# Optimization experiments

Hardware: AMD Instinct MI355X
Metric: run time of the kernel (lower is better)

## Reference

```python
import jax, jax.numpy as jnp
import numpy as np

V = 32          # number_variables
DEG = 12        # degree
ORDER = 3       # spline_order (cubic)
N_BASIS = DEG + ORDER - 1  # 14, rows of params
LO, HI = -15.0, 15.0       # polynomial_range[:, 0]
EPS = 1e-6


def make_knots():
    dist = (HI - LO) / (DEG - 1)
    k = DEG + 2 * ORDER
    return jnp.linspace(LO - ORDER * dist, HI + ORDER * dist, k, dtype=jnp.float32)


def bspline_basis(x, knots, order):
    # x: [N, P] -> basis: [N, P, N_BASIS] via Cox-de Boor recursion (Naive_Basis)
    xk = x[..., None]
    b = ((xk >= knots[:-1]) & (xk < knots[1:])).astype(x.dtype)  # degree-0, [N,P,K-1]
    t = knots
    for k in range(1, order + 1):
        left = (xk - t[:-(k + 1)]) / (t[k:-1] - t[:-(k + 1)])
        right = (t[k + 1:] - xk) / (t[k + 1:] - t[1:-k])
        b = left * b[..., :-1] + right * b[..., 1:]
    return b  # [N, P, K-1-order] == [N, P, N_BASIS]


def setup_inputs() -> dict:
    key = jax.random.key(0)
    k1, k2 = jax.random.split(key)
    num_lambdas = V * (V - 1) // 2  # 496
    inp = jax.random.normal(k1, (16384, V), dtype=jnp.float32)
    log_d = jnp.zeros((16384, V), dtype=jnp.float32)
    params = 0.001 * jnp.ones((N_BASIS, num_lambdas), dtype=jnp.float32)
    return {"input": inp, "log_d": log_d, "params": params}


def reference(input, log_d, params):
    n = input.shape[0]
    knots = make_knots()
    rows, cols = np.tril_indices(V, -1)  # matches torch.tril_indices(V, V, offset=-1)
    rows = jnp.asarray(rows); cols = jnp.asarray(cols)
    # clamp into half-open spline support for valid degree-0 basis
    x = jnp.clip(input, LO, HI - EPS)
    xs = x[:, cols]                                  # [N, P] per-pair covariate values
    basis = bspline_basis(xs, knots, ORDER)          # [N, P, N_BASIS]
    lam = jnp.einsum('npk,kp->np', basis, params)    # [N, P] lambda values
    # lower-triangular lambda matrix: identity + strict lower entries
    lm = jnp.broadcast_to(jnp.eye(V, dtype=input.dtype), (n, V, V))
    lm = lm.at[:, rows, cols].set(lam)
    out = jnp.einsum('nvc,nc->nv', lm, input)        # bmm(lambda_matrix, input)
    # ridge penalties on spline coefficients (penalize_towards=0)
    d2 = jnp.diff(params, n=2, axis=0)
    d1 = jnp.diff(params, n=1, axis=0)
    second_pen = jnp.sum(d2 ** 2)
    first_pen = jnp.sum(d1 ** 2)
    param_pen = jnp.sum(params ** 2)
    return out, lm, second_pen, first_pen, param_pen
```

## Files before the change

kernel.cpp:

```cpp
#include <hip/hip_runtime.h>

#define VDIM   32
#define NPAIR  496
#define NBASIS 14
#define NPARAM (NBASIS * NPAIR)
#define ROWS   16
#define SPS    15

typedef float f32x4 __attribute__((ext_vector_type(4)));

__device__ __forceinline__ float spline_u(float xi) {
    const float invd = 11.0f / 30.0f;
    float x = fminf(fmaxf(xi, -15.0f), 15.0f - 1e-6f);
    return x * invd + 8.5f;
}

__global__ __launch_bounds__(256) void Decorrelation_35270271435435_kernel(
    const float* __restrict__ input,
    const float* __restrict__ params,
    float* __restrict__ out,
    float* __restrict__ lm,
    float* __restrict__ pens,
    int N)
{
    __shared__ float sp[NPAIR * SPS];
    __shared__ float xin[ROWS][VDIM];
    __shared__ f32x4 wgt4[ROWS][VDIM];

    const int tid = threadIdx.x;
    const int n0  = blockIdx.x * ROWS;

    {
        const f32x4* p4 = (const f32x4*)params;
        for (int i4 = tid; i4 < NPARAM / 4; i4 += 256) {
            const f32x4 val = p4[i4];
            const int base = i4 * 4;
            #pragma unroll
            for (int e = 0; e < 4; ++e) {
                const int idx = base + e;
                const int k = idx / NPAIR;
                const int p = idx - k * NPAIR;
                sp[p * SPS + k] = val[e];
            }
        }
    }

    #pragma unroll
    for (int it = 0; it < 2; ++it) {
        const int item = tid + it * 256;
        const int r = item >> 5, c = item & 31;
        const int n = n0 + r;
        const float xi = (n < N) ? input[n * VDIM + c] : 0.0f;
        xin[r][c] = xi;
        const float u  = spline_u(xi);
        float fi = floorf(u);
        fi = fminf(fmaxf(fi, 3.0f), 13.0f);
        const float uu  = u - fi;
        const float om  = 1.0f - uu;
        const float uu2 = uu * uu, uu3 = uu2 * uu;
        const float sixth = 1.0f / 6.0f;
        f32x4 w;
        w[0] = om * om * om * sixth;
        w[1] = (3.0f * uu3 - 6.0f * uu2 + 4.0f) * sixth;
        w[2] = (-3.0f * uu3 + 3.0f * uu2 + 3.0f * uu + 1.0f) * sixth;
        w[3] = uu3 * sixth;
        wgt4[r][((c & 3) << 3) | (c >> 2)] = w;
    }
    __syncthreads();

    const int v  = tid >> 3;
    const int t  = tid & 7;
    const int c0 = t << 2;
    int  pb[4];
    bool low[4], dia[4];
    #pragma unroll
    for (int j = 0; j < 4; ++j) {
        const int c = c0 + j;
        low[j] = (c < v);
        dia[j] = (c == v);
        pb[j]  = ((v * (v - 1)) / 2 + c) * SPS;
    }

    const int rlim = (N - n0 < ROWS) ? (N - n0) : ROWS;
    float* lmp = lm + (size_t)n0 * (VDIM * VDIM) + tid * 4;

    #pragma unroll 4
    for (int r = 0; r < ROWS; ++r, lmp += VDIM * VDIM) {
        const f32x4 x4 = *(const f32x4*)&xin[r][c0];
        float vals[4];
        float partial = 0.0f;
        #pragma unroll
        for (int j = 0; j < 4; ++j) {
            float val = 0.0f;
            if (dia[j]) {
                val = 1.0f;
            } else if (low[j]) {
                const float u = spline_u(x4[j]);
                float fi = floorf(u);
                fi = fminf(fmaxf(fi, 3.0f), 13.0f);
                const int k0 = (int)fi - 3;
                const float* q = &sp[pb[j] + k0];
                const f32x4 w = wgt4[r][(j << 3) | t];
                val = w[0] * q[0] + w[1] * q[1] + w[2] * q[2] + w[3] * q[3];
            }
            vals[j] = val;
            partial += val * x4[j];
        }
        if (r < rlim) {
            const f32x4 f4 = { vals[0], vals[1], vals[2], vals[3] };
            __builtin_nontemporal_store(f4, (f32x4*)lmp);
            partial += __shfl_down(partial, 4, 8);
            partial += __shfl_down(partial, 2, 8);
            partial += __shfl_down(partial, 1, 8);
            if (t == 0) out[(size_t)(n0 + r) * VDIM + v] = partial;
        }
    }

    if (blockIdx.x == 0) {
        float s2 = 0.0f, s1 = 0.0f, spn = 0.0f;
        for (int p = tid; p < NPAIR; p += 256) {
            const float* q = &sp[p * SPS];
            float a[NBASIS];
            #pragma unroll
            for (int k = 0; k < NBASIS; ++k) { a[k] = q[k]; spn += a[k] * a[k]; }
            #pragma unroll
            for (int k = 0; k < NBASIS - 1; ++k) {
                const float d = a[k + 1] - a[k];
                s1 += d * d;
            }
            #pragma unroll
            for (int k = 0; k < NBASIS - 2; ++k) {
                const float d = a[k + 2] - 2.0f * a[k + 1] + a[k];
                s2 += d * d;
            }
        }
        #pragma unroll
        for (int off = 32; off > 0; off >>= 1) {
            s2  += __shfl_down(s2, off);
            s1  += __shfl_down(s1, off);
            spn += __shfl_down(spn, off);
        }
        __shared__ float wsum[3][4];
        const int lane = tid & 63, wid = tid >> 6;
        if (lane == 0) { wsum[0][wid] = s2; wsum[1][wid] = s1; wsum[2][wid] = spn; }
        __syncthreads();
        if (tid == 0) {
            pens[0] = wsum[0][0] + wsum[0][1] + wsum[0][2] + wsum[0][3];
            pens[1] = wsum[1][0] + wsum[1][1] + wsum[1][2] + wsum[1][3];
            pens[2] = wsum[2][0] + wsum[2][1] + wsum[2][2] + wsum[2][3];
        }
    }
}

extern "C" void kernel_launch(void* const* d_in, const int* in_sizes, int n_in,
                              void* d_out, int out_size, void* d_ws, size_t ws_size,
                              hipStream_t stream) {
    const float* input  = (const float*)d_in[0];
    const float* params = (const float*)d_in[2];
    const int N = in_sizes[0] / VDIM;

    float* out  = (float*)d_out;
    float* lm   = out + (size_t)N * VDIM;
    float* pens = lm + (size_t)N * VDIM * VDIM;

    const int nb = (N + ROWS - 1) / ROWS;
    Decorrelation_35270271435435_kernel<<<nb, 256, 0, stream>>>(
        input, params, out, lm, pens, N);
}
```

Measured before the change: 89.79 us.

## Double block size and compute spline weights inline per element

Blocks grow to 512 threads, so two row groups work on interleaved rows and each thread handles half as many rows. The shared-memory staging of inputs and precomputed cubic B-spline weights is removed. Each thread now reads its input row directly from global memory and computes the weights in registers, which drops one LDS pass and its associated buffers. The cost is redundant weight computation and an unchanged per-block params load into shared memory. That load is now amortised over fewer rows per thread but shared across more threads.

Result: slower. 92.66 us (+3.2%).

```diff
diff --git a/kernel.cpp b/kernel.cpp
--- a/kernel.cpp
+++ b/kernel.cpp
@@ -5,6 +5,7 @@
 #define NBASIS 14
 #define NPARAM (NBASIS * NPAIR)
 #define ROWS   16
+#define BLK    512
 #define SPS    15
 
 typedef float f32x4 __attribute__((ext_vector_type(4)));
@@ -15,7 +16,7 @@
     return x * invd + 8.5f;
 }
 
-__global__ __launch_bounds__(256) void Decorrelation_35270271435435_kernel(
+__global__ __launch_bounds__(BLK, 8) void Decorrelation_35270271435435_kernel(
     const float* __restrict__ input,
     const float* __restrict__ params,
     float* __restrict__ out,
@@ -24,15 +25,14 @@
     int N)
 {
     __shared__ float sp[NPAIR * SPS];
-    __shared__ float xin[ROWS][VDIM];
-    __shared__ f32x4 wgt4[ROWS][VDIM];
+    __shared__ float wsum[3][8];
 
     const int tid = threadIdx.x;
     const int n0  = blockIdx.x * ROWS;
 
     {
         const f32x4* p4 = (const f32x4*)params;
-        for (int i4 = tid; i4 < NPARAM / 4; i4 += 256) {
+        for (int i4 = tid; i4 < NPARAM / 4; i4 += BLK) {
             const f32x4 val = p4[i4];
             const int base = i4 * 4;
             #pragma unroll
@@ -44,31 +44,10 @@
             }
         }
     }
-
-    #pragma unroll
-    for (int it = 0; it < 2; ++it) {
-        const int item = tid + it * 256;
-        const int r = item >> 5, c = item & 31;
-        const int n = n0 + r;
-        const float xi = (n < N) ? input[n * VDIM + c] : 0.0f;
-        xin[r][c] = xi;
-        const float u  = spline_u(xi);
-        float fi = floorf(u);
-        fi = fminf(fmaxf(fi, 3.0f), 13.0f);
-        const float uu  = u - fi;
-        const float om  = 1.0f - uu;
-        const float uu2 = uu * uu, uu3 = uu2 * uu;
-        const float sixth = 1.0f / 6.0f;
-        f32x4 w;
-        w[0] = om * om * om * sixth;
-        w[1] = (3.0f * uu3 - 6.0f * uu2 + 4.0f) * sixth;
-        w[2] = (-3.0f * uu3 + 3.0f * uu2 + 3.0f * uu + 1.0f) * sixth;
-        w[3] = uu3 * sixth;
-        wgt4[r][((c & 3) << 3) | (c >> 2)] = w;
-    }
     __syncthreads();
 
-    const int v  = tid >> 3;
+    const int g  = tid >> 8;
+    const int v  = (tid >> 3) & 31;
     const int t  = tid & 7;
     const int c0 = t << 2;
     int  pb[4];
@@ -81,12 +60,14 @@
         pb[j]  = ((v * (v - 1)) / 2 + c) * SPS;
     }
 
-    const int rlim = (N - n0 < ROWS) ? (N - n0) : ROWS;
-    float* lmp = lm + (size_t)n0 * (VDIM * VDIM) + tid * 4;
+    float* lmp0 = lm + (size_t)(n0 + g) * (VDIM * VDIM) + (tid & 255) * 4;
 
-    #pragma unroll 4
-    for (int r = 0; r < ROWS; ++r, lmp += VDIM * VDIM) {
-        const f32x4 x4 = *(const f32x4*)&xin[r][c0];
+    #pragma unroll 2
+    for (int i = 0; i < ROWS / 2; ++i) {
+        const int r = g + (i << 1);
+        const int n = n0 + r;
+        if (n >= N) break;
+        const f32x4 x4 = *(const f32x4*)&input[(size_t)n * VDIM + c0];
         float vals[4];
         float partial = 0.0f;
         #pragma unroll
@@ -98,27 +79,33 @@
                 const float u = spline_u(x4[j]);
                 float fi = floorf(u);
                 fi = fminf(fmaxf(fi, 3.0f), 13.0f);
+                const float uu  = u - fi;
+                const float om  = 1.0f - uu;
+                const float uu2 = uu * uu, uu3 = uu2 * uu;
+                const float sixth = 1.0f / 6.0f;
+                const float w0 = om * om * om * sixth;
+                const float w1 = (3.0f * uu3 - 6.0f * uu2 + 4.0f) * sixth;
+                const float w2 = (-3.0f * uu3 + 3.0f * uu2 + 3.0f * uu + 1.0f) * sixth;
+                const float w3 = uu3 * sixth;
                 const int k0 = (int)fi - 3;
                 const float* q = &sp[pb[j] + k0];
-                const f32x4 w = wgt4[r][(j << 3) | t];
-                val = w[0] * q[0] + w[1] * q[1] + w[2] * q[2] + w[3] * q[3];
+                val = w0 * q[0] + w1 * q[1] + w2 * q[2] + w3 * q[3];
             }
             vals[j] = val;
             partial += val * x4[j];
         }
-        if (r < rlim) {
-            const f32x4 f4 = { vals[0], vals[1], vals[2], vals[3] };
-            __builtin_nontemporal_store(f4, (f32x4*)lmp);
-            partial += __shfl_down(partial, 4, 8);
-            partial += __shfl_down(partial, 2, 8);
-            partial += __shfl_down(partial, 1, 8);
-            if (t == 0) out[(size_t)(n0 + r) * VDIM + v] = partial;
-        }
+        const f32x4 f4 = { vals[0], vals[1], vals[2], vals[3] };
+        __builtin_nontemporal_store(f4, (f32x4*)(lmp0 + (size_t)(i << 1) * (VDIM * VDIM)));
+
+        partial += __shfl_down(partial, 4, 8);
+        partial += __shfl_down(partial, 2, 8);
+        partial += __shfl_down(partial, 1, 8);
+        if (t == 0) out[(size_t)n * VDIM + v] = partial;
     }
 
     if (blockIdx.x == 0) {
         float s2 = 0.0f, s1 = 0.0f, spn = 0.0f;
-        for (int p = tid; p < NPAIR; p += 256) {
+        for (int p = tid; p < NPAIR; p += BLK) {
             const float* q = &sp[p * SPS];
             float a[NBASIS];
             #pragma unroll
@@ -140,14 +127,14 @@
             s1  += __shfl_down(s1, off);
             spn += __shfl_down(spn, off);
         }
-        __shared__ float wsum[3][4];
         const int lane = tid & 63, wid = tid >> 6;
         if (lane == 0) { wsum[0][wid] = s2; wsum[1][wid] = s1; wsum[2][wid] = spn; }
         __syncthreads();
         if (tid == 0) {
-            pens[0] = wsum[0][0] + wsum[0][1] + wsum[0][2] + wsum[0][3];
-            pens[1] = wsum[1][0] + wsum[1][1] + wsum[1][2] + wsum[1][3];
-            pens[2] = wsum[2][0] + wsum[2][1] + wsum[2][2] + wsum[2][3];
+            float r0 = 0.f, r1 = 0.f, r2 = 0.f;
+            #pragma unroll
+            for (int w = 0; w < 8; ++w) { r0 += wsum[0][w]; r1 += wsum[1][w]; r2 += wsum[2][w]; }
+            pens[0] = r0; pens[1] = r1; pens[2] = r2;
         }
     }
 }
@@ -164,6 +151,6 @@
     float* pens = lm + (size_t)N * VDIM * VDIM;
 
     const int nb = (N + ROWS - 1) / ROWS;
-    Decorrelation_35270271435435_kernel<<<nb, 256, 0, stream>>>(
+    Decorrelation_35270271435435_kernel<<<nb, BLK, 0, stream>>>(
         input, params, out, lm, pens, N);
 }
```
